# Optimization experiments

Measured on AMD Instinct MI355X. Metric: run time of the kernel, lower is better.

## Reference

```python
import jax, jax.numpy as jnp
import numpy as np

D = 1024  # d_model

def setup_inputs() -> dict:
    key = jax.random.key(0)
    ks = jax.random.split(key, 12)
    s = 1.0 / np.sqrt(D)  # torch Linear default init scale
    inp = {
        "q": jax.random.normal(ks[0], (4, 4096, D), dtype=jnp.float32),
        "k": jax.random.normal(ks[1], (4, 4096, D), dtype=jnp.float32),
        "v": jax.random.normal(ks[2], (4, 4096, D), dtype=jnp.float32),
        "Wq": jax.random.uniform(ks[3], (D, D), jnp.float32, -s, s),
        "bq": jax.random.uniform(ks[4], (D,), jnp.float32, -s, s),
        "Wk": jax.random.uniform(ks[5], (D, D), jnp.float32, -s, s),
        "bk": jax.random.uniform(ks[6], (D,), jnp.float32, -s, s),
        "Wv": jax.random.uniform(ks[7], (D, D), jnp.float32, -s, s),
        "bv": jax.random.uniform(ks[8], (D,), jnp.float32, -s, s),
        "Wo": jax.random.uniform(ks[9], (D, D), jnp.float32, -s, s),
        "bo": jax.random.uniform(ks[10], (D,), jnp.float32, -s, s),
    }
    return inp

def reference(q, k, v, Wq, bq, Wk, bk, Wv, bv, Wo, bo):
    # phi feature map: exp(-x^2 / 2)
    phi = lambda x: jnp.exp(-0.5 * x * x)
    Q = phi(q @ Wq.T + bq)            # [B, N, D]
    K = phi(k @ Wk.T + bk)            # [B, N, D]
    V = v @ Wv.T + bv                 # [B, N, D]
    # linear attention: aggregate K^T V once, then contract with Q
    KV = jnp.einsum('bnd,bnl->bdl', K, V)                 # [B, D, D]
    Z = 1.0 / (jnp.einsum('bnd,bd->bn', Q, K.sum(axis=1)) + 1e-6)  # [B, N]
    out = jnp.einsum('bnd,bdl->bnl', Q, KV) * Z[..., None]         # [B, N, D]
    return out @ Wo.T + bo
```

## Files before the change

### kernel.cpp

```cpp
#include <hip/hip_runtime.h>

typedef unsigned short u16;
typedef unsigned int u32;
typedef unsigned long long u64;

typedef __attribute__((ext_vector_type(8))) short short8;
typedef __attribute__((ext_vector_type(4))) float floatx4;

__device__ __forceinline__ float b2f(u16 h) {
  u32 u = ((u32)h) << 16;
  return __builtin_bit_cast(float, u);
}
__device__ __forceinline__ u16 f2b(float f) {
  u32 u = __builtin_bit_cast(u32, f);
  u32 r = 0x7FFFu + ((u >> 16) & 1u);
  return (u16)((u + r) >> 16);
}

__device__ __forceinline__ void gl_lds16(const void* g, void* l) {
  __builtin_amdgcn_global_load_lds(
      (__attribute__((address_space(1))) void*)(u64)g,
      (__attribute__((address_space(3))) void*)(u32)(u64)l, 16, 0, 0);
}

enum { EPI_PHI_BIAS = 0, EPI_BIAS = 1, EPI_NONE = 2,
       EPI_ZBIAS_F32 = 3 };

template<int EPI, bool TRANS_OUT>
__global__ __launch_bounds__(512, 2)
void gemm_bt256(const u16* __restrict__ Ap, const u16* __restrict__ Bp0,
                const float* __restrict__ bias, const float* __restrict__ Zall,
                void* __restrict__ Cp,
                int M, int N, int K, int ldA, int ldB, int ldC,
                long sAb, long sBb, long sCb, long sZb, int abmask, int kshift)
{
  constexpr int BSTRIDE = 32768;
  constexpr int BOFF    = 16384;
  __shared__ char smem[3 * BSTRIDE];

  const int tid  = threadIdx.x;
  const int lane = tid & 63;
  const int wave = tid >> 6;
  const int wm = wave >> 2, wn = wave & 3;
  const int fl = lane & 15;
  const int q  = lane >> 4;
  const int r4 = q * 4;
  const int bm0 = blockIdx.x * 256, bn0 = blockIdx.y * 256;
  const int bz = blockIdx.z;
  const int abz = bz & abmask;
  const int kbase = (bz >> kshift) * K;

  const u16* Ah = Ap  + (size_t)abz * sAb + kbase;
  const u16* Bh = Bp0 + (size_t)abz * sBb + kbase;

  const u16* gA[2]; const u16* gB[2]; int sL[2];
  #pragma unroll
  for (int n = 0; n < 2; ++n) {
    int j = n * 512 + tid;
    int R = j >> 3, u = (j & 7) ^ (R & 7);
    int r = (R << 1) | (u >> 2), c = u & 3;
    gA[n] = Ah + (size_t)(bm0 + r) * ldA + c * 8;
    gB[n] = Bh + (size_t)(bn0 + r) * ldB + c * 8;
    sL[n] = (n * 512 + wave * 64) * 16;
  }

  int aoff[8], boff[4];
  #pragma unroll
  for (int i = 0; i < 8; ++i) {
    int ra = wm * 128 + i * 16 + fl;
    int Ra = ra >> 1, ua = ((((ra & 1) << 2) | q) ^ (Ra & 7));
    aoff[i] = (Ra * 8 + ua) * 16;
  }
  #pragma unroll
  for (int i = 0; i < 4; ++i) {
    int rb = wn * 64 + i * 16 + fl;
    int Rb = rb >> 1, ub = ((((rb & 1) << 2) | q) ^ (Rb & 7));
    boff[i] = (Rb * 8 + ub) * 16;
  }

  floatx4 zero = {0.f, 0.f, 0.f, 0.f};
  floatx4 acc[8][4];
  #pragma unroll
  for (int i = 0; i < 8; ++i)
    #pragma unroll
    for (int j = 0; j < 4; ++j) acc[i][j] = zero;

  auto stage = [&](int k0, char* base) {
    #pragma unroll
    for (int n = 0; n < 2; ++n) gl_lds16(gA[n] + k0, base + sL[n]);
    #pragma unroll
    for (int n = 0; n < 2; ++n) gl_lds16(gB[n] + k0, base + BOFF + sL[n]);
  };

  auto kstep = [&](const char* bufc) {
    short8 bF[4], aF[8];
    #pragma unroll
    for (int i = 0; i < 4; ++i) bF[i] = *(const short8*)(bufc + BOFF + boff[i]);
    #pragma unroll
    for (int i = 0; i < 8; ++i) aF[i] = *(const short8*)(bufc + aoff[i]);
    __builtin_amdgcn_s_setprio(1);
    #pragma unroll
    for (int mi = 0; mi < 8; ++mi)
      #pragma unroll
      for (int ni = 0; ni < 4; ++ni)
        acc[mi][ni] = __builtin_amdgcn_mfma_f32_16x16x32_bf16(
            aF[mi], bF[ni], acc[mi][ni], 0, 0, 0);
    __builtin_amdgcn_s_setprio(0);
  };

  const int NIT = K >> 5;
  stage(0, smem);
  stage(32, smem + BSTRIDE);
  asm volatile("s_waitcnt vmcnt(4)\ns_barrier" ::: "memory");
  int c0 = 0, c2 = 2 * BSTRIDE;
  for (int n = 0; n < NIT; ++n) {
    bool pf = n + 2 < NIT;
    if (pf) stage((n + 2) * 32, smem + c2);
    kstep(smem + c0);
    if (n + 1 < NIT) {
      if (pf) asm volatile("s_waitcnt vmcnt(4) lgkmcnt(0)\ns_barrier" ::: "memory");
      else    asm volatile("s_waitcnt vmcnt(0) lgkmcnt(0)\ns_barrier" ::: "memory");
    }
    c0 = c0 == 2 * BSTRIDE ? 0 : c0 + BSTRIDE;
    c2 = c2 == 2 * BSTRIDE ? 0 : c2 + BSTRIDE;
  }

  if constexpr (!TRANS_OUT) {
    #pragma unroll
    for (int mi = 0; mi < 8; ++mi) {
      #pragma unroll
      for (int ni = 0; ni < 4; ++ni) {
        int col = bn0 + wn * 64 + ni * 16 + fl;
        #pragma unroll
        for (int r = 0; r < 4; ++r) {
          int row = bm0 + wm * 128 + mi * 16 + r4 + r;
          float vv = acc[mi][ni][r];
          if constexpr (EPI == EPI_PHI_BIAS) {
            vv += bias[col];
            vv = __expf(-0.5f * vv * vv);
          }
          if constexpr (EPI == EPI_ZBIAS_F32)
            vv = vv * Zall[(size_t)abz * sZb + row] + bias[col];
          if constexpr (EPI == EPI_ZBIAS_F32)
            ((float*)Cp)[(size_t)bz * sCb + (size_t)row * ldC + col] = vv;
          else
            ((u16*)Cp)[(size_t)bz * sCb + (size_t)row * ldC + col] = f2b(vv);
        }
      }
    }
  } else {
    u16* sT = (u16*)smem;
    #pragma unroll
    for (int p = 0; p < 2; ++p) {
      __syncthreads();
      if ((wn >> 1) == p) {
        #pragma unroll
        for (int mi = 0; mi < 8; ++mi) {
          #pragma unroll
          for (int ni = 0; ni < 4; ++ni) {
            int colL = wn * 64 + ni * 16 + fl;
            int row0 = wm * 128 + mi * 16 + r4;
            float bcol = bias[bn0 + colL];
            ushort4 h;
            #pragma unroll
            for (int r = 0; r < 4; ++r) {
              float vv = acc[mi][ni][r] + bcol;
              if constexpr (EPI == EPI_PHI_BIAS) vv = __expf(-0.5f * vv * vv);
              ((u16*)&h)[r] = f2b(vv);
            }
            *(ushort4*)(sT + (colL - p * 128) * 264 + row0) = h;
          }
        }
      }
      __syncthreads();
      #pragma unroll
      for (int i = 0; i < 8; ++i) {
        int c = tid + i * 512;
        int dloc = c >> 5, t8 = (c & 31) * 8;
        int4 vv = *(const int4*)(sT + dloc * 264 + t8);
        int gd = bn0 + p * 128 + dloc;
        int gt = bm0 + t8;
        int batch = gt >> 12, tt = gt & 4095;
        *(int4*)((u16*)Cp + ((size_t)batch * N + gd) * 4096 + tt) = vv;
      }
    }
  }
}

__global__ __launch_bounds__(256)
void fcvt(const float* __restrict__ src, u16* __restrict__ dst) {
  size_t i = ((size_t)blockIdx.x * 256 + threadIdx.x) * 8;
  float4 a = *(const float4*)(src + i);
  float4 b = *(const float4*)(src + i + 4);
  union { ushort4 h[2]; int4 v; } o;
  o.h[0].x = f2b(a.x); o.h[0].y = f2b(a.y); o.h[0].z = f2b(a.z); o.h[0].w = f2b(a.w);
  o.h[1].x = f2b(b.x); o.h[1].y = f2b(b.y); o.h[1].z = f2b(b.z); o.h[1].w = f2b(b.w);
  *(int4*)(dst + i) = o.v;
}

__global__ __launch_bounds__(256)
void wconv(const float* __restrict__ w0, const float* __restrict__ w1,
           const float* __restrict__ w2, const float* __restrict__ w3,
           u16* __restrict__ dst) {
  unsigned e = blockIdx.x * 256 + threadIdx.x;
  int mat = e >> 18;
  size_t off = (size_t)(e & 262143) * 4;
  const float* src = mat == 0 ? w0 : mat == 1 ? w1 : mat == 2 ? w2 : w3;
  float4 v = *(const float4*)(src + off);
  ushort4 h;
  h.x = f2b(v.x); h.y = f2b(v.y); h.z = f2b(v.z); h.w = f2b(v.w);
  *(ushort4*)(dst + (size_t)mat * 1048576 + off) = h;
}

__global__ __launch_bounds__(256)
void reduce4(const u16* __restrict__ P, u16* __restrict__ out) {
  size_t i = ((size_t)blockIdx.x * 256 + threadIdx.x) * 8;
  int4 a = *(const int4*)(P + i);
  int4 b = *(const int4*)(P + i + 4194304);
  int4 c = *(const int4*)(P + i + 8388608);
  int4 d = *(const int4*)(P + i + 12582912);
  const u16* ha = (const u16*)&a; const u16* hb = (const u16*)&b;
  const u16* hc = (const u16*)&c; const u16* hd = (const u16*)&d;
  ushort4 o0, o1;
  #pragma unroll
  for (int j = 0; j < 8; ++j) {
    float s = b2f(ha[j]) + b2f(hb[j]) + b2f(hc[j]) + b2f(hd[j]);
    ((u16*)(j < 4 ? &o0 : &o1))[j & 3] = f2b(s);
  }
  *(ushort4*)(out + i) = o0;
  *(ushort4*)(out + i + 4) = o1;
}

__global__ __launch_bounds__(256)
void ksum_rows(const u16* __restrict__ KT, float* __restrict__ Ksum) {
  int lane = threadIdx.x & 63;
  int row = blockIdx.x * 4 + (threadIdx.x >> 6);
  const u16* p = KT + (size_t)row * 4096;
  float s = 0.f;
  #pragma unroll
  for (int i = 0; i < 8; ++i) {
    int4 d = *(const int4*)(p + i * 512 + lane * 8);
    const u16* h = (const u16*)&d;
    #pragma unroll
    for (int j = 0; j < 8; ++j) s += b2f(h[j]);
  }
  #pragma unroll
  for (int off = 32; off; off >>= 1) s += __shfl_xor(s, off, 64);
  if (lane == 0) Ksum[row] = s;
}

__global__ __launch_bounds__(256)
void zden(const u16* __restrict__ Qb, const float* __restrict__ Ksum,
          float* __restrict__ Z) {
  int lane = threadIdx.x & 63;
  int t = blockIdx.x * 4 + (threadIdx.x >> 6);
  const u16* qp = Qb + (size_t)t * 1024;
  const float* ks = Ksum + (size_t)(t >> 12) * 1024;
  float s = 0.f;
  #pragma unroll
  for (int i = 0; i < 2; ++i) {
    int idx = i * 512 + lane * 8;
    int4 d = *(const int4*)(qp + idx);
    const u16* h = (const u16*)&d;
    float4 k0 = *(const float4*)(ks + idx);
    float4 k1 = *(const float4*)(ks + idx + 4);
    s += b2f(h[0]) * k0.x + b2f(h[1]) * k0.y + b2f(h[2]) * k0.z + b2f(h[3]) * k0.w
       + b2f(h[4]) * k1.x + b2f(h[5]) * k1.y + b2f(h[6]) * k1.z + b2f(h[7]) * k1.w;
  }
  #pragma unroll
  for (int off = 32; off; off >>= 1) s += __shfl_xor(s, off, 64);
  if (lane == 0) Z[t] = 1.0f / (s + 1e-6f);
}

extern "C" void kernel_launch(void* const* d_in, const int* in_sizes, int n_in,
                              void* d_out, int out_size, void* d_ws, size_t ws_size,
                              hipStream_t stream) {
  const float* q  = (const float*)d_in[0];
  const float* k  = (const float*)d_in[1];
  const float* v  = (const float*)d_in[2];
  const float* Wq = (const float*)d_in[3];
  const float* bq = (const float*)d_in[4];
  const float* Wk = (const float*)d_in[5];
  const float* bk = (const float*)d_in[6];
  const float* Wv = (const float*)d_in[7];
  const float* bv = (const float*)d_in[8];
  const float* Wo = (const float*)d_in[9];
  const float* bo = (const float*)d_in[10];
  float* out = (float*)d_out;

  u16* Wqb = (u16*)d_ws;
  u16* Wkb = Wqb + 1048576;
  u16* Wvb = Wkb + 1048576;
  u16* Wob = Wvb + 1048576;
  u16* Qb  = Wob + 1048576;
  u16* KT  = Qb  + 16777216;
  u16* VT  = KT  + 16777216;
  u16* KVr = VT  + 16777216;
  float* Ksum = (float*)(KVr + 4194304);
  float* Z    = Ksum + 4096;
  u16* kb16 = Qb;
  u16* vb16 = Qb;
  u16* Pkv  = Qb;
  u16* Pg   = VT;
  u16* Gp   = KT;
  u16* qb16 = VT;

  wconv<<<4096, 256, 0, stream>>>(Wq, Wk, Wv, Wo, Wqb);
  fcvt<<<8192, 256, 0, stream>>>(k, kb16);

  dim3 gp(64, 4, 1);
  gemm_bt256<EPI_PHI_BIAS, true><<<gp, 512, 0, stream>>>(
      kb16, Wkb, bk, nullptr, KT, 16384, 1024, 1024, 1024, 1024, 0,
      0, 0, 0, 0, 0, 2);
  ksum_rows<<<1024, 256, 0, stream>>>(KT, Ksum);

  fcvt<<<8192, 256, 0, stream>>>(v, vb16);
  gemm_bt256<EPI_BIAS, true><<<gp, 512, 0, stream>>>(
      vb16, Wvb, bv, nullptr, VT, 16384, 1024, 1024, 1024, 1024, 0,
      0, 0, 0, 0, 0, 2);

  dim3 g2(4, 4, 16);
  gemm_bt256<EPI_NONE, false><<<g2, 512, 0, stream>>>(
      KT, VT, nullptr, nullptr, Pkv, 1024, 1024, 1024, 4096, 4096, 1024,
      4194304L, 4194304L, 1048576L, 0, 3, 2);
  reduce4<<<2048, 256, 0, stream>>>(Pkv, KVr);

  dim3 gg(4, 4, 16);
  gemm_bt256<EPI_NONE, false><<<gg, 512, 0, stream>>>(
      Wob, KVr, nullptr, nullptr, Pg, 1024, 1024, 256, 1024, 1024, 1024,
      0L, 1048576L, 1048576L, 0, 3, 2);
  reduce4<<<2048, 256, 0, stream>>>(Pg, Gp);

  fcvt<<<8192, 256, 0, stream>>>(q, qb16);
  gemm_bt256<EPI_PHI_BIAS, false><<<gp, 512, 0, stream>>>(
      qb16, Wqb, bq, nullptr, Qb, 16384, 1024, 1024, 1024, 1024, 1024,
      0, 0, 0, 0, 0, 2);
  zden<<<4096, 256, 0, stream>>>(Qb, Ksum, Z);

  dim3 gf(16, 4, 4);
  gemm_bt256<EPI_ZBIAS_F32, false><<<gf, 512, 0, stream>>>(
      Qb, Gp, bo, Z, out, 4096, 1024, 1024, 1024, 1024, 1024,
      4194304L, 1048576L, 4194304L, 4096L, 3, 2);
}
```

Measured before the change: 309.8 us.

## Switch GEMM to double-buffered K=64 tiles with two MFMA substeps per barrier

Replaces the triple-buffered K=32 LDS pipeline with a double-buffered K=64 pipeline. Each tile now holds 256 rows of 128 bytes with an XOR swizzle, and the two 32-wide halves are selected by XOR-ing the read offset. This halves the number of barriers and waitcnt points per K, cutting synchronisation overhead. In exchange it prefetches only one tile ahead and waits for vmcnt(0), so less memory latency is hidden, and it raises LDS to 128KB per block, which may limit how many blocks fit per CU.

New measurement: 301.2 us. -2.8%, faster.

```diff
diff --git a/kernel.cpp b/kernel.cpp
--- a/kernel.cpp
+++ b/kernel.cpp
@@ -34,9 +34,9 @@
                 int M, int N, int K, int ldA, int ldB, int ldC,
                 long sAb, long sBb, long sCb, long sZb, int abmask, int kshift)
 {
-  constexpr int BSTRIDE = 32768;
-  constexpr int BOFF    = 16384;
-  __shared__ char smem[3 * BSTRIDE];
+  constexpr int TSTRIDE = 65536;
+  constexpr int BOFF    = 32768;
+  __shared__ char smem[2 * TSTRIDE];
 
   const int tid  = threadIdx.x;
   const int lane = tid & 63;
@@ -53,14 +53,13 @@
   const u16* Ah = Ap  + (size_t)abz * sAb + kbase;
   const u16* Bh = Bp0 + (size_t)abz * sBb + kbase;
 
-  const u16* gA[2]; const u16* gB[2]; int sL[2];
-  #pragma unroll
-  for (int n = 0; n < 2; ++n) {
+  const u16* gA[4]; const u16* gB[4]; int sL[4];
+  #pragma unroll
+  for (int n = 0; n < 4; ++n) {
     int j = n * 512 + tid;
-    int R = j >> 3, u = (j & 7) ^ (R & 7);
-    int r = (R << 1) | (u >> 2), c = u & 3;
-    gA[n] = Ah + (size_t)(bm0 + r) * ldA + c * 8;
-    gB[n] = Bh + (size_t)(bn0 + r) * ldB + c * 8;
+    int R = j >> 3, c = (j & 7) ^ (R & 7);
+    gA[n] = Ah + (size_t)(bm0 + R) * ldA + c * 8;
+    gB[n] = Bh + (size_t)(bn0 + R) * ldB + c * 8;
     sL[n] = (n * 512 + wave * 64) * 16;
   }
 
@@ -68,14 +67,12 @@
   #pragma unroll
   for (int i = 0; i < 8; ++i) {
     int ra = wm * 128 + i * 16 + fl;
-    int Ra = ra >> 1, ua = ((((ra & 1) << 2) | q) ^ (Ra & 7));
-    aoff[i] = (Ra * 8 + ua) * 16;
+    aoff[i] = ra * 128 + ((q ^ (ra & 7)) * 16);
   }
   #pragma unroll
   for (int i = 0; i < 4; ++i) {
     int rb = wn * 64 + i * 16 + fl;
-    int Rb = rb >> 1, ub = ((((rb & 1) << 2) | q) ^ (Rb & 7));
-    boff[i] = (Rb * 8 + ub) * 16;
+    boff[i] = rb * 128 + ((q ^ (rb & 7)) * 16);
   }
 
   floatx4 zero = {0.f, 0.f, 0.f, 0.f};
@@ -85,19 +82,20 @@
     #pragma unroll
     for (int j = 0; j < 4; ++j) acc[i][j] = zero;
 
-  auto stage = [&](int k0, char* base) {
-    #pragma unroll
-    for (int n = 0; n < 2; ++n) gl_lds16(gA[n] + k0, base + sL[n]);
-    #pragma unroll
-    for (int n = 0; n < 2; ++n) gl_lds16(gB[n] + k0, base + BOFF + sL[n]);
+  auto stage = [&](int t, char* base) {
+    int k0 = t * 64;
+    #pragma unroll
+    for (int n = 0; n < 4; ++n) gl_lds16(gA[n] + k0, base + sL[n]);
+    #pragma unroll
+    for (int n = 0; n < 4; ++n) gl_lds16(gB[n] + k0, base + BOFF + sL[n]);
   };
 
-  auto kstep = [&](const char* bufc) {
+  auto kstep = [&](const char* bufc, int xo) {
     short8 bF[4], aF[8];
     #pragma unroll
-    for (int i = 0; i < 4; ++i) bF[i] = *(const short8*)(bufc + BOFF + boff[i]);
-    #pragma unroll
-    for (int i = 0; i < 8; ++i) aF[i] = *(const short8*)(bufc + aoff[i]);
+    for (int i = 0; i < 4; ++i) bF[i] = *(const short8*)(bufc + BOFF + (boff[i] ^ xo));
+    #pragma unroll
+    for (int i = 0; i < 8; ++i) aF[i] = *(const short8*)(bufc + (aoff[i] ^ xo));
     __builtin_amdgcn_s_setprio(1);
     #pragma unroll
     for (int mi = 0; mi < 8; ++mi)
@@ -108,21 +106,18 @@
     __builtin_amdgcn_s_setprio(0);
   };
 
-  const int NIT = K >> 5;
+  const int NT = K >> 6;
   stage(0, smem);
-  stage(32, smem + BSTRIDE);
-  asm volatile("s_waitcnt vmcnt(4)\ns_barrier" ::: "memory");
-  int c0 = 0, c2 = 2 * BSTRIDE;
-  for (int n = 0; n < NIT; ++n) {
-    bool pf = n + 2 < NIT;
-    if (pf) stage((n + 2) * 32, smem + c2);
-    kstep(smem + c0);
-    if (n + 1 < NIT) {
-      if (pf) asm volatile("s_waitcnt vmcnt(4) lgkmcnt(0)\ns_barrier" ::: "memory");
-      else    asm volatile("s_waitcnt vmcnt(0) lgkmcnt(0)\ns_barrier" ::: "memory");
-    }
-    c0 = c0 == 2 * BSTRIDE ? 0 : c0 + BSTRIDE;
-    c2 = c2 == 2 * BSTRIDE ? 0 : c2 + BSTRIDE;
+  asm volatile("s_waitcnt vmcnt(0)\ns_barrier" ::: "memory");
+  int cur = 0;
+  for (int t = 0; t < NT; ++t) {
+    if (t + 1 < NT) stage(t + 1, smem + (cur ^ TSTRIDE));
+    const char* bufc = smem + cur;
+    kstep(bufc, 0);
+    kstep(bufc, 64);
+    if (t + 1 < NT)
+      asm volatile("s_waitcnt vmcnt(0) lgkmcnt(0)\ns_barrier" ::: "memory");
+    cur ^= TSTRIDE;
   }
 
   if constexpr (!TRANS_OUT) {
```
